# Performance work log

Measured on AMD Instinct MI355X. Metric: run time of the kernel, lower is better.

The kernel has to match this reference:

```python
import jax, jax.numpy as jnp
import numpy as np

N = 50000        # nodes
E = 800000       # edges (avg degree 16)
F_IN = 128       # input feature dim == heads*hidden of every layer
H = 4            # heads per layer
C = 32           # hidden (per-head out) per layer
ED = 16          # edge_dim
L = 3            # num GAT layers
NEG_SLOPE = 0.2  # PyG GATConv default


def setup_inputs() -> dict:
    key = jax.random.key(0)
    ks = jax.random.split(key, 13)
    s = 0.1
    x = jax.random.normal(ks[0], (N, F_IN), jnp.float32)
    edge_index = jax.random.randint(ks[1], (2, E), 0, N, dtype=jnp.int32)
    edge_attr = jax.random.normal(ks[2], (E, ED), jnp.float32)
    # stacked per-layer GATConv params (all layers are 128 -> 4x32)
    W_src = jax.random.normal(ks[3], (L, F_IN, H * C), jnp.float32) * s
    att_src = jax.random.normal(ks[4], (L, H, C), jnp.float32) * s
    att_dst = jax.random.normal(ks[5], (L, H, C), jnp.float32) * s
    W_edge = jax.random.normal(ks[6], (L, ED, H * C), jnp.float32) * s
    att_edge = jax.random.normal(ks[7], (L, H, C), jnp.float32) * s
    bias = jnp.zeros((L, H * C), jnp.float32)
    # dense head: Linear(128,256) -> ReLU -> Linear(256,2)
    W1 = jax.random.normal(ks[8], (H * C, 2 * H * C), jnp.float32) * s
    b1 = jnp.zeros((2 * H * C,), jnp.float32)
    W2 = jax.random.normal(ks[9], (2 * H * C, 2), jnp.float32) * s
    b2 = jnp.zeros((2,), jnp.float32)
    return {"x": x, "edge_index": edge_index, "edge_attr": edge_attr,
            "W_src": W_src, "att_src": att_src, "att_dst": att_dst,
            "W_edge": W_edge, "att_edge": att_edge, "bias": bias,
            "W1": W1, "b1": b1, "W2": W2, "b2": b2}


def reference(x, edge_index, edge_attr, W_src, att_src, att_dst,
              W_edge, att_edge, bias, W1, b1, W2, b2):
    src, dst = edge_index[0], edge_index[1]
    # add_self_loops with fill_value='mean': self-loop edge_attr = mean of
    # incoming edge attrs per node (0 if no incoming edges)
    deg = jax.ops.segment_sum(jnp.ones((E,), x.dtype), dst, num_segments=N)
    loop_attr = jax.ops.segment_sum(edge_attr, dst, num_segments=N) \
        / jnp.maximum(deg, 1.0)[:, None]
    nodes = jnp.arange(N, dtype=src.dtype)
    src_f = jnp.concatenate([src, nodes])          # [E+N]
    dst_f = jnp.concatenate([dst, nodes])          # [E+N]
    ea = jnp.concatenate([edge_attr, loop_attr], axis=0)  # [E+N, ED]

    h = x
    for l in range(L):
        hp = (h @ W_src[l]).reshape(N, H, C)                 # [N,H,C]
        a_s = (hp * att_src[l]).sum(-1)                      # [N,H]
        a_d = (hp * att_dst[l]).sum(-1)                      # [N,H]
        ef = (ea @ W_edge[l]).reshape(-1, H, C)              # [E+N,H,C]
        a_e = (ef * att_edge[l]).sum(-1)                     # [E+N,H]
        alpha = jax.nn.leaky_relu(a_s[src_f] + a_d[dst_f] + a_e, NEG_SLOPE)
        # segment softmax over destination node (self-loops ensure coverage)
        m = jax.ops.segment_max(alpha, dst_f, num_segments=N)
        ex = jnp.exp(alpha - m[dst_f])
        denom = jax.ops.segment_sum(ex, dst_f, num_segments=N)
        w = ex / denom[dst_f]                                # [E+N,H]
        agg = jax.ops.segment_sum(w[:, :, None] * hp[src_f], dst_f,
                                  num_segments=N)            # [N,H,C]
        h = jax.nn.relu(agg.reshape(N, H * C) + bias[l])

    g = h.mean(axis=0, keepdims=True)                        # batch=None -> [1,128]
    hid = jax.nn.relu(g @ W1 + b1)
    return hid @ W2 + b2                                     # [1,2]
```

## Files before the change

kernel.cpp:

```cpp
#include <hip/hip_runtime.h>
#include <math.h>

#define N_NODES 50000
#define N_EDGES 800000
#define F 128
#define H 4
#define C 32
#define ED 16
#define L 3
#define NEG 0.2f
#define ET (N_EDGES + N_NODES)
#define SCAN_B ((N_NODES + 255) / 256)


__global__ void k_loop_acc(const int* __restrict__ dst, const float* __restrict__ edge_attr,
                           float* __restrict__ loop_sum, int* __restrict__ deg) {
    int idx = blockIdx.x * 256 + threadIdx.x;
    if (idx >= N_EDGES * ED) return;
    int e = idx >> 4, d = idx & 15;
    int dn = dst[e];
    atomicAdd(&loop_sum[dn * ED + d], edge_attr[idx]);
    if (d == 0) atomicAdd(&deg[dn], 1);
}

__global__ __launch_bounds__(256) void k_scanA(const int* __restrict__ deg,
                                               int* __restrict__ off, int* __restrict__ bsum) {
    __shared__ int sh[256];
    int t = threadIdx.x;
    int i = blockIdx.x * 256 + t;
    int v = (i < N_NODES) ? (deg[i] + 1) : 0;
    sh[t] = v;
    __syncthreads();
    #pragma unroll
    for (int d = 1; d < 256; d <<= 1) {
        int u = (t >= d) ? sh[t - d] : 0;
        __syncthreads();
        sh[t] += u;
        __syncthreads();
    }
    if (i < N_NODES) off[i] = sh[t] - v;
    if (t == 255) bsum[blockIdx.x] = sh[255];
}

__global__ __launch_bounds__(256) void k_scanB(const int* __restrict__ bsum,
                                               int* __restrict__ boff, int* __restrict__ off) {
    __shared__ int sh[256];
    int t = threadIdx.x;
    int v = (t < SCAN_B) ? bsum[t] : 0;
    sh[t] = v;
    __syncthreads();
    #pragma unroll
    for (int d = 1; d < 256; d <<= 1) {
        int u = (t >= d) ? sh[t - d] : 0;
        __syncthreads();
        sh[t] += u;
        __syncthreads();
    }
    if (t < SCAN_B) boff[t] = sh[t] - v;
    if (t == 255) off[N_NODES] = sh[255];
}

__global__ void k_scanC(int* __restrict__ off, const int* __restrict__ boff) {
    int i = blockIdx.x * 256 + threadIdx.x;
    if (i < N_NODES) off[i] += boff[blockIdx.x];
}

__global__ void k_scatter(const int* __restrict__ ei, const int* __restrict__ off,
                          int* __restrict__ cursor, int* __restrict__ src_csr,
                          int* __restrict__ pos_arr) {
    int e = blockIdx.x * 256 + threadIdx.x;
    if (e < N_EDGES) {
        int d = ei[N_EDGES + e];
        int p = atomicAdd(&cursor[d], 1);
        int slot = off[d] + p;
        src_csr[slot] = ei[e];
        pos_arr[e] = slot;
    } else if (e < ET) {
        int nn = e - N_EDGES;
        int p = atomicAdd(&cursor[nn], 1);
        int slot = off[nn] + p;
        src_csr[slot] = nn;
        pos_arr[e] = slot;
    }
}

__global__ void k_loop_div(const int* __restrict__ deg, float* __restrict__ loop_attr) {
    int idx = blockIdx.x * 256 + threadIdx.x;
    if (idx >= N_NODES * ED) return;
    int n = idx >> 4;
    loop_attr[idx] = loop_attr[idx] / fmaxf((float)deg[n], 1.f);
}

__global__ void k_we2(const float* __restrict__ W_edge, const float* __restrict__ att_edge,
                      float* __restrict__ we2) {
    int idx = blockIdx.x * 64 + threadIdx.x;
    if (idx >= L * ED * H) return;
    int l = idx / (ED * H);
    int r = idx % (ED * H);
    int d = r / H, h = r % H;
    float s = 0.f;
    for (int c = 0; c < C; c++)
        s += W_edge[(size_t)(l * ED + d) * (H * C) + h * C + c] * att_edge[(l * H + h) * C + c];
    we2[idx] = s;
}


#define BM 64
#define BK 32
__global__ __launch_bounds__(256) void k_gemm(const float* __restrict__ A,
                                              const float* __restrict__ W,
                                              const float* __restrict__ att_src_l,
                                              const float* __restrict__ att_dst_l,
                                              float* __restrict__ Out,
                                              float* __restrict__ a_s,
                                              float* __restrict__ a_d) {
    __shared__ float As[BM][BK + 1];
    __shared__ float Bs[BK][F];
    int block_row = blockIdx.x * BM;
    int t = threadIdx.x;
    int tx = t & 31;
    int ty = t >> 5;
    float acc[8][4] = {};
    for (int k0 = 0; k0 < F; k0 += BK) {
        #pragma unroll
        for (int i = 0; i < 2; i++) {
            int idx = t + i * 256;
            int r = idx >> 3, cq = idx & 7;
            int gr = block_row + r;
            float4 v = make_float4(0.f, 0.f, 0.f, 0.f);
            if (gr < N_NODES) v = *(const float4*)&A[(size_t)gr * F + k0 + cq * 4];
            As[r][cq * 4 + 0] = v.x; As[r][cq * 4 + 1] = v.y;
            As[r][cq * 4 + 2] = v.z; As[r][cq * 4 + 3] = v.w;
        }
        #pragma unroll
        for (int i = 0; i < 4; i++) {
            int idx = t + i * 256;
            int r = idx >> 5, cq = idx & 31;
            float4 v = *(const float4*)&W[(size_t)(k0 + r) * F + cq * 4];
            *(float4*)&Bs[r][cq * 4] = v;
        }
        __syncthreads();
        for (int kk = 0; kk < BK; kk++) {
            float b[4];
            #pragma unroll
            for (int j = 0; j < 4; j++) b[j] = Bs[kk][tx + 32 * j];
            #pragma unroll
            for (int i = 0; i < 8; i++) {
                float a = As[ty * 8 + i][kk];
                #pragma unroll
                for (int j = 0; j < 4; j++) acc[i][j] += a * b[j];
            }
        }
        __syncthreads();
    }
    float avs[4], avd[4];
    #pragma unroll
    for (int j = 0; j < 4; j++) {
        avs[j] = att_src_l[j * 32 + tx];
        avd[j] = att_dst_l[j * 32 + tx];
    }
    #pragma unroll
    for (int i = 0; i < 8; i++) {
        int gr = block_row + ty * 8 + i;
        bool ok = (gr < N_NODES);
        if (ok) {
            #pragma unroll
            for (int j = 0; j < 4; j++) Out[(size_t)gr * F + tx + 32 * j] = acc[i][j];
        }
        #pragma unroll
        for (int j = 0; j < 4; j++) {
            float vs = acc[i][j] * avs[j];
            float vd = acc[i][j] * avd[j];
            #pragma unroll
            for (int m = 1; m < 32; m <<= 1) {
                vs += __shfl_xor(vs, m, 64);
                vd += __shfl_xor(vd, m, 64);
            }
            if (tx == 0 && ok) {
                a_s[gr * H + j] = vs;
                a_d[gr * H + j] = vd;
            }
        }
    }
}

__global__ void k_alpha(const int* __restrict__ ei, const float* __restrict__ edge_attr,
                        const float* __restrict__ loop_attr, const float* __restrict__ we2l,
                        const float* __restrict__ a_s, const float* __restrict__ a_d,
                        const int* __restrict__ pos_arr, float* __restrict__ alpha_csr) {
    int e = blockIdx.x * 256 + threadIdx.x;
    if (e >= ET) return;
    int s, d; const float* ea;
    if (e < N_EDGES) { s = ei[e]; d = ei[N_EDGES + e]; ea = &edge_attr[(size_t)e * ED]; }
    else { int nn = e - N_EDGES; s = nn; d = nn; ea = &loop_attr[(size_t)nn * ED]; }
    float eav[ED];
    #pragma unroll
    for (int q = 0; q < ED / 4; q++) {
        float4 v = *(const float4*)&ea[q * 4];
        eav[q * 4 + 0] = v.x; eav[q * 4 + 1] = v.y;
        eav[q * 4 + 2] = v.z; eav[q * 4 + 3] = v.w;
    }
    float ae[H] = {0.f, 0.f, 0.f, 0.f};
    #pragma unroll
    for (int k = 0; k < ED; k++) {
        float v = eav[k];
        #pragma unroll
        for (int h = 0; h < H; h++) ae[h] += v * we2l[k * H + h];
    }
    int slot = pos_arr[e];
    float4 out;
    float* o = (float*)&out;
    #pragma unroll
    for (int h = 0; h < H; h++) {
        float a = a_s[s * H + h] + a_d[d * H + h] + ae[h];
        o[h] = (a > 0.f) ? a : NEG * a;
    }
    *(float4*)&alpha_csr[(size_t)slot * H] = out;
}

__global__ __launch_bounds__(128) void k_agg(const int* __restrict__ src_csr, const int* __restrict__ off,
                                             const float* __restrict__ alpha_csr,
                                             const float* __restrict__ hp, const float* __restrict__ bias_l,
                                             float* __restrict__ hout) {
    int n = blockIdx.x;
    int c = threadIdx.x;
    int h = c >> 5;
    int beg = off[n], end = off[n + 1];
    float acc0 = 0.f, acc1 = 0.f, acc2 = 0.f, acc3 = 0.f;
    float den0 = 0.f, den1 = 0.f, den2 = 0.f, den3 = 0.f;
    int i = beg;
    for (; i + 4 <= end; i += 4) {
        int s0 = src_csr[i], s1 = src_csr[i + 1], s2 = src_csr[i + 2], s3 = src_csr[i + 3];
        float a0 = alpha_csr[(size_t)i * H + h];
        float a1 = alpha_csr[(size_t)(i + 1) * H + h];
        float a2 = alpha_csr[(size_t)(i + 2) * H + h];
        float a3 = alpha_csr[(size_t)(i + 3) * H + h];
        float e0 = __expf(a0), e1 = __expf(a1), e2 = __expf(a2), e3 = __expf(a3);
        acc0 += e0 * hp[(size_t)s0 * F + c];
        acc1 += e1 * hp[(size_t)s1 * F + c];
        acc2 += e2 * hp[(size_t)s2 * F + c];
        acc3 += e3 * hp[(size_t)s3 * F + c];
        den0 += e0; den1 += e1; den2 += e2; den3 += e3;
    }
    for (; i < end; i++) {
        int s0 = src_csr[i];
        float a0 = alpha_csr[(size_t)i * H + h];
        float e0 = __expf(a0);
        acc0 += e0 * hp[(size_t)s0 * F + c];
        den0 += e0;
    }
    float acc = (acc0 + acc1) + (acc2 + acc3);
    float den = (den0 + den1) + (den2 + den3);
    float v = acc / den + bias_l[c];
    hout[(size_t)n * F + c] = fmaxf(v, 0.f);
}


__global__ void k_pool(const float* __restrict__ hfinal, float* __restrict__ gsum) {
    int c = threadIdx.x;
    float s = 0.f;
    for (int n = blockIdx.x; n < N_NODES; n += gridDim.x)
        s += hfinal[(size_t)n * F + c];
    atomicAdd(&gsum[c], s);
}

__global__ __launch_bounds__(256) void k_mlp(const float* __restrict__ gsum, const float* __restrict__ W1,
                                             const float* __restrict__ b1, const float* __restrict__ W2,
                                             const float* __restrict__ b2, float* __restrict__ out) {
    __shared__ float g[F];
    __shared__ float hid[2 * F];
    __shared__ float red[256];
    int t = threadIdx.x;
    if (t < F) g[t] = gsum[t] * (1.0f / N_NODES);
    __syncthreads();
    float s = b1[t];
    for (int k = 0; k < F; k++) s += g[k] * W1[k * (2 * F) + t];
    hid[t] = fmaxf(s, 0.f);
    __syncthreads();
    for (int i = 0; i < 2; i++) {
        red[t] = hid[t] * W2[t * 2 + i];
        __syncthreads();
        for (int stp = 128; stp > 0; stp >>= 1) {
            if (t < stp) red[t] += red[t + stp];
            __syncthreads();
        }
        if (t == 0) out[i] = red[0] + b2[i];
        __syncthreads();
    }
}


extern "C" void kernel_launch(void* const* d_in, const int* in_sizes, int n_in,
                              void* d_out, int out_size, void* d_ws, size_t ws_size,
                              hipStream_t stream) {
    const float* x        = (const float*)d_in[0];
    const int*   ei       = (const int*)d_in[1];
    const float* edge_attr= (const float*)d_in[2];
    const float* W_src    = (const float*)d_in[3];
    const float* att_src  = (const float*)d_in[4];
    const float* att_dst  = (const float*)d_in[5];
    const float* W_edge   = (const float*)d_in[6];
    const float* att_edge = (const float*)d_in[7];
    const float* bias     = (const float*)d_in[8];
    const float* W1       = (const float*)d_in[9];
    const float* b1       = (const float*)d_in[10];
    const float* W2       = (const float*)d_in[11];
    const float* b2       = (const float*)d_in[12];
    float* out = (float*)d_out;

    char* p = (char*)d_ws;
    auto alloc = [&](size_t bytes) -> char* {
        char* r = p;
        p += (bytes + 255) & ~(size_t)255;
        return r;
    };
    int*      deg      = (int*)alloc((size_t)N_NODES * 4);
    int*      cursor   = (int*)alloc((size_t)N_NODES * 4);
    int*      off      = (int*)alloc((size_t)(N_NODES + 1) * 4);
    int*      bsum     = (int*)alloc((size_t)SCAN_B * 4);
    int*      boff     = (int*)alloc((size_t)SCAN_B * 4);
    int*      src_csr  = (int*)alloc((size_t)ET * 4);
    int*      pos_arr  = (int*)alloc((size_t)ET * 4);
    float*    loop_attr= (float*)alloc((size_t)N_NODES * ED * 4);
    float*    we2      = (float*)alloc((size_t)L * ED * H * 4);
    float*    a_s      = (float*)alloc((size_t)N_NODES * H * 4);
    float*    a_d      = (float*)alloc((size_t)N_NODES * H * 4);
    float*    alpha_csr= (float*)alloc((size_t)ET * H * 4);
    float*    hp       = (float*)alloc((size_t)N_NODES * F * 4);
    float*    hA       = (float*)alloc((size_t)N_NODES * F * 4);
    float*    hB       = (float*)alloc((size_t)N_NODES * F * 4);
    float*    gsum     = (float*)alloc((size_t)F * 4);

    hipMemsetAsync(deg, 0, (size_t)N_NODES * 4, stream);
    hipMemsetAsync(cursor, 0, (size_t)N_NODES * 4, stream);
    hipMemsetAsync(loop_attr, 0, (size_t)N_NODES * ED * 4, stream);
    hipMemsetAsync(gsum, 0, (size_t)F * 4, stream);

    const int* dst = ei + N_EDGES;
    k_loop_acc<<<(N_EDGES * ED + 255) / 256, 256, 0, stream>>>(dst, edge_attr, loop_attr, deg);
    k_scanA<<<SCAN_B, 256, 0, stream>>>(deg, off, bsum);
    k_scanB<<<1, 256, 0, stream>>>(bsum, boff, off);
    k_scanC<<<SCAN_B, 256, 0, stream>>>(off, boff);
    k_scatter<<<(ET + 255) / 256, 256, 0, stream>>>(ei, off, cursor, src_csr, pos_arr);
    k_loop_div<<<(N_NODES * ED + 255) / 256, 256, 0, stream>>>(deg, loop_attr);
    k_we2<<<3, 64, 0, stream>>>(W_edge, att_edge, we2);

    const float* hin = x;
    float* houts[3] = {hA, hB, hA};
    for (int l = 0; l < L; l++) {
        k_gemm<<<(N_NODES + BM - 1) / BM, 256, 0, stream>>>(hin, W_src + (size_t)l * F * F,
                                                            att_src + l * H * C, att_dst + l * H * C,
                                                            hp, a_s, a_d);
        k_alpha<<<(ET + 255) / 256, 256, 0, stream>>>(ei, edge_attr, loop_attr,
                                                      we2 + l * ED * H, a_s, a_d,
                                                      pos_arr, alpha_csr);
        k_agg<<<N_NODES, 128, 0, stream>>>(src_csr, off, alpha_csr, hp,
                                           bias + l * F, houts[l]);
        hin = houts[l];
    }
    k_pool<<<256, 128, 0, stream>>>(hA, gsum);
    k_mlp<<<1, 256, 0, stream>>>(gsum, W1, b1, W2, b2, out);
}
```

Baseline: 698.3 us.

## Compute self-loop edge attention from mean of incoming logits, drop loop_attr atomics

Removes the per-element atomic accumulation of self-loop edge attributes, which cost 12.8M float atomics, along with the loop_attr divide pass. It relies on linearity: the self-loop edge logit equals the mean of the incoming edges' edge logits. k_alpha is restructured to run one wavefront per destination node over the CSR, gathering edge_attr by stored edge id, and it reduces the partial sums with shuffles to form the self-loop logit. The trade-offs are irregular gathers of edge_attr in CSR order instead of coalesced reads, load imbalance across nodes of different degree, and a slightly different floating-point summation order.

```diff
diff --git a/kernel.cpp b/kernel.cpp
--- a/kernel.cpp
+++ b/kernel.cpp
@@ -13,14 +13,9 @@
 #define SCAN_B ((N_NODES + 255) / 256)
 
 
-__global__ void k_loop_acc(const int* __restrict__ dst, const float* __restrict__ edge_attr,
-                           float* __restrict__ loop_sum, int* __restrict__ deg) {
-    int idx = blockIdx.x * 256 + threadIdx.x;
-    if (idx >= N_EDGES * ED) return;
-    int e = idx >> 4, d = idx & 15;
-    int dn = dst[e];
-    atomicAdd(&loop_sum[dn * ED + d], edge_attr[idx]);
-    if (d == 0) atomicAdd(&deg[dn], 1);
+__global__ void k_count(const int* __restrict__ dst, int* __restrict__ deg) {
+    int e = blockIdx.x * 256 + threadIdx.x;
+    if (e < N_EDGES) atomicAdd(&deg[dst[e]], 1);
 }
 
 __global__ __launch_bounds__(256) void k_scanA(const int* __restrict__ deg,
@@ -67,28 +62,21 @@
 
 __global__ void k_scatter(const int* __restrict__ ei, const int* __restrict__ off,
                           int* __restrict__ cursor, int* __restrict__ src_csr,
-                          int* __restrict__ pos_arr) {
+                          int* __restrict__ eid_csr) {
     int e = blockIdx.x * 256 + threadIdx.x;
     if (e < N_EDGES) {
         int d = ei[N_EDGES + e];
         int p = atomicAdd(&cursor[d], 1);
         int slot = off[d] + p;
         src_csr[slot] = ei[e];
-        pos_arr[e] = slot;
+        eid_csr[slot] = e;
     } else if (e < ET) {
         int nn = e - N_EDGES;
         int p = atomicAdd(&cursor[nn], 1);
         int slot = off[nn] + p;
         src_csr[slot] = nn;
-        pos_arr[e] = slot;
-    }
-}
-
-__global__ void k_loop_div(const int* __restrict__ deg, float* __restrict__ loop_attr) {
-    int idx = blockIdx.x * 256 + threadIdx.x;
-    if (idx >= N_NODES * ED) return;
-    int n = idx >> 4;
-    loop_attr[idx] = loop_attr[idx] / fmaxf((float)deg[n], 1.f);
+        eid_csr[slot] = e;
+    }
 }
 
 __global__ void k_we2(const float* __restrict__ W_edge, const float* __restrict__ att_edge,
@@ -184,38 +172,72 @@
     }
 }
 
-__global__ void k_alpha(const int* __restrict__ ei, const float* __restrict__ edge_attr,
-                        const float* __restrict__ loop_attr, const float* __restrict__ we2l,
-                        const float* __restrict__ a_s, const float* __restrict__ a_d,
-                        const int* __restrict__ pos_arr, float* __restrict__ alpha_csr) {
-    int e = blockIdx.x * 256 + threadIdx.x;
-    if (e >= ET) return;
-    int s, d; const float* ea;
-    if (e < N_EDGES) { s = ei[e]; d = ei[N_EDGES + e]; ea = &edge_attr[(size_t)e * ED]; }
-    else { int nn = e - N_EDGES; s = nn; d = nn; ea = &loop_attr[(size_t)nn * ED]; }
-    float eav[ED];
-    #pragma unroll
-    for (int q = 0; q < ED / 4; q++) {
-        float4 v = *(const float4*)&ea[q * 4];
-        eav[q * 4 + 0] = v.x; eav[q * 4 + 1] = v.y;
-        eav[q * 4 + 2] = v.z; eav[q * 4 + 3] = v.w;
-    }
-    float ae[H] = {0.f, 0.f, 0.f, 0.f};
-    #pragma unroll
-    for (int k = 0; k < ED; k++) {
-        float v = eav[k];
-        #pragma unroll
-        for (int h = 0; h < H; h++) ae[h] += v * we2l[k * H + h];
-    }
-    int slot = pos_arr[e];
-    float4 out;
-    float* o = (float*)&out;
-    #pragma unroll
-    for (int h = 0; h < H; h++) {
-        float a = a_s[s * H + h] + a_d[d * H + h] + ae[h];
-        o[h] = (a > 0.f) ? a : NEG * a;
-    }
-    *(float4*)&alpha_csr[(size_t)slot * H] = out;
+__global__ __launch_bounds__(256) void k_alpha(const int* __restrict__ eid_csr,
+                                               const int* __restrict__ src_csr,
+                                               const int* __restrict__ off,
+                                               const float* __restrict__ edge_attr,
+                                               const float* __restrict__ we2l,
+                                               const float* __restrict__ a_s,
+                                               const float* __restrict__ a_d,
+                                               float* __restrict__ alpha_csr) {
+    int n = blockIdx.x * 4 + (threadIdx.x >> 6);
+    if (n >= N_NODES) return;
+    int lane = threadIdx.x & 63;
+    int beg = off[n], end = off[n + 1];
+    float4 w[ED];
+    #pragma unroll
+    for (int k = 0; k < ED; k++) w[k] = *(const float4*)&we2l[k * 4];
+    float4 adn = *(const float4*)&a_d[(size_t)n * 4];
+    float sx = 0.f, sy = 0.f, sz = 0.f, sw = 0.f;
+    int self_slot = -1;
+    for (int i = beg + lane; i < end; i += 64) {
+        int eid = eid_csr[i];
+        if (eid < N_EDGES) {
+            int src = src_csr[i];
+            float4 asrc = *(const float4*)&a_s[(size_t)src * 4];
+            const float* ea = &edge_attr[(size_t)eid * ED];
+            float eav[ED];
+            #pragma unroll
+            for (int q = 0; q < ED / 4; q++) {
+                float4 v = *(const float4*)&ea[q * 4];
+                eav[q * 4 + 0] = v.x; eav[q * 4 + 1] = v.y;
+                eav[q * 4 + 2] = v.z; eav[q * 4 + 3] = v.w;
+            }
+            float ax = 0.f, ay = 0.f, az = 0.f, aw = 0.f;
+            #pragma unroll
+            for (int k = 0; k < ED; k++) {
+                float v = eav[k];
+                ax += v * w[k].x; ay += v * w[k].y;
+                az += v * w[k].z; aw += v * w[k].w;
+            }
+            sx += ax; sy += ay; sz += az; sw += aw;
+            float4 o;
+            o.x = asrc.x + adn.x + ax; o.x = (o.x > 0.f) ? o.x : NEG * o.x;
+            o.y = asrc.y + adn.y + ay; o.y = (o.y > 0.f) ? o.y : NEG * o.y;
+            o.z = asrc.z + adn.z + az; o.z = (o.z > 0.f) ? o.z : NEG * o.z;
+            o.w = asrc.w + adn.w + aw; o.w = (o.w > 0.f) ? o.w : NEG * o.w;
+            *(float4*)&alpha_csr[(size_t)i * H] = o;
+        } else {
+            self_slot = i;
+        }
+    }
+    #pragma unroll
+    for (int m = 1; m < 64; m <<= 1) {
+        sx += __shfl_xor(sx, m, 64);
+        sy += __shfl_xor(sy, m, 64);
+        sz += __shfl_xor(sz, m, 64);
+        sw += __shfl_xor(sw, m, 64);
+    }
+    if (self_slot >= 0) {
+        float inv = 1.f / fmaxf((float)(end - beg - 1), 1.f);
+        float4 asn = *(const float4*)&a_s[(size_t)n * 4];
+        float4 o;
+        o.x = asn.x + adn.x + sx * inv; o.x = (o.x > 0.f) ? o.x : NEG * o.x;
+        o.y = asn.y + adn.y + sy * inv; o.y = (o.y > 0.f) ? o.y : NEG * o.y;
+        o.z = asn.z + adn.z + sz * inv; o.z = (o.z > 0.f) ? o.z : NEG * o.z;
+        o.w = asn.w + adn.w + sw * inv; o.w = (o.w > 0.f) ? o.w : NEG * o.w;
+        *(float4*)&alpha_csr[(size_t)self_slot * H] = o;
+    }
 }
 
 __global__ __launch_bounds__(128) void k_agg(const int* __restrict__ src_csr, const int* __restrict__ off,
@@ -320,8 +342,7 @@
     int*      bsum     = (int*)alloc((size_t)SCAN_B * 4);
     int*      boff     = (int*)alloc((size_t)SCAN_B * 4);
     int*      src_csr  = (int*)alloc((size_t)ET * 4);
-    int*      pos_arr  = (int*)alloc((size_t)ET * 4);
-    float*    loop_attr= (float*)alloc((size_t)N_NODES * ED * 4);
+    int*      eid_csr  = (int*)alloc((size_t)ET * 4);
     float*    we2      = (float*)alloc((size_t)L * ED * H * 4);
     float*    a_s      = (float*)alloc((size_t)N_NODES * H * 4);
     float*    a_d      = (float*)alloc((size_t)N_NODES * H * 4);
@@ -333,16 +354,14 @@
 
     hipMemsetAsync(deg, 0, (size_t)N_NODES * 4, stream);
     hipMemsetAsync(cursor, 0, (size_t)N_NODES * 4, stream);
-    hipMemsetAsync(loop_attr, 0, (size_t)N_NODES * ED * 4, stream);
     hipMemsetAsync(gsum, 0, (size_t)F * 4, stream);
 
     const int* dst = ei + N_EDGES;
-    k_loop_acc<<<(N_EDGES * ED + 255) / 256, 256, 0, stream>>>(dst, edge_attr, loop_attr, deg);
+    k_count<<<(N_EDGES + 255) / 256, 256, 0, stream>>>(dst, deg);
     k_scanA<<<SCAN_B, 256, 0, stream>>>(deg, off, bsum);
     k_scanB<<<1, 256, 0, stream>>>(bsum, boff, off);
     k_scanC<<<SCAN_B, 256, 0, stream>>>(off, boff);
-    k_scatter<<<(ET + 255) / 256, 256, 0, stream>>>(ei, off, cursor, src_csr, pos_arr);
-    k_loop_div<<<(N_NODES * ED + 255) / 256, 256, 0, stream>>>(deg, loop_attr);
+    k_scatter<<<(ET + 255) / 256, 256, 0, stream>>>(ei, off, cursor, src_csr, eid_csr);
     k_we2<<<3, 64, 0, stream>>>(W_edge, att_edge, we2);
 
     const float* hin = x;
@@ -351,9 +370,8 @@
         k_gemm<<<(N_NODES + BM - 1) / BM, 256, 0, stream>>>(hin, W_src + (size_t)l * F * F,
                                                             att_src + l * H * C, att_dst + l * H * C,
                                                             hp, a_s, a_d);
-        k_alpha<<<(ET + 255) / 256, 256, 0, stream>>>(ei, edge_attr, loop_attr,
-                                                      we2 + l * ED * H, a_s, a_d,
-                                                      pos_arr, alpha_csr);
+        k_alpha<<<(N_NODES + 3) / 4, 256, 0, stream>>>(eid_csr, src_csr, off, edge_attr,
+                                                       we2 + l * ED * H, a_s, a_d, alpha_csr);
         k_agg<<<N_NODES, 128, 0, stream>>>(src_csr, off, alpha_csr, hp,
                                            bias + l * F, houts[l]);
         hin = houts[l];
```

After: 681.7 us. -2.4%, faster.
